# Kernel tuning notes

Hardware: AMD Instinct MI355X
Metric: run time of the kernel (lower is better)

## Reference

```python
import jax, jax.numpy as jnp
import numpy as np
import math

NEG_INF = -1e9  # stand-in for Const.NegInf
D_QKV = 64

def setup_inputs() -> dict:
    key = jax.random.key(0)
    kq, kk, kv, km = jax.random.split(key, 4)
    B, H, S, D = 4, 16, 2048, D_QKV
    q = jax.random.normal(kq, (B, H, S, D), dtype=jnp.float32)
    k = jax.random.normal(kk, (B, H, S, D), dtype=jnp.float32)
    v = jax.random.normal(kv, (B, H, S, D), dtype=jnp.float32)
    mask = jax.random.randint(km, (1, 1, S, S), 0, 2, dtype=jnp.int32)
    return {"q": q, "k": k, "v": v, "mask": mask, "batch": B, "q_seq": S}

def reference(q, k, v, mask, batch, q_seq):
    # scores: (B, H, Sq, Sk)
    scores = jnp.einsum('bhqd,bhkd->bhqk', q, k) / math.sqrt(D_QKV)
    # NOTE: non-standard order (faithful to source): log_softmax FIRST,
    # (dropout skipped since dropout_rate == 0), THEN post-softmax masking.
    score = jax.nn.log_softmax(scores, axis=-1)
    score = jnp.where(mask == 0, jnp.asarray(NEG_INF, score.dtype), score)
    att = jnp.einsum('bhqk,bhkd->bhqd', score, v)
    # (B, H, Sq, D) -> (B, Sq, H*D)
    return att.transpose(0, 2, 1, 3).reshape(batch, q_seq, -1)
```

## Files before the change

kernel.cpp:

```cpp
#include <hip/hip_runtime.h>

#define S_LEN 2048

typedef __attribute__((ext_vector_type(8))) short bf16x8;
typedef __attribute__((ext_vector_type(4))) float f32x4;
typedef __attribute__((ext_vector_type(4))) unsigned int u32x4;
typedef unsigned long long u64;
typedef unsigned int u32;
typedef unsigned short u16;

#define MFMA16 __builtin_amdgcn_mfma_f32_16x16x32_bf16

__device__ __forceinline__ u32 cvtpk(float a, float b) {
  u32 r;
  asm("v_cvt_pk_bf16_f32 %0, %1, %2" : "=v"(r) : "v"(a), "v"(b));
  return r;
}
__device__ __forceinline__ float exp2hw(float x) {
  float r;
  asm("v_exp_f32 %0, %1" : "=v"(r) : "v"(x));
  return r;
}

__device__ __forceinline__ u64* qkaddr(u16* dst, int row, int c4) {
  const int cb = c4 >> 1;
  return (u64*)((char*)dst + ((((row << 3) + (cb ^ (row & 7))) << 4) + ((c4 & 1) << 3)));
}
__device__ __forceinline__ bf16x8 ldfrag(const u16* base, int row, int blk) {
  const char* p = (const char*)base + (((row << 3) + (blk ^ (row & 7))) << 4);
  return *(const bf16x8*)p;
}

__device__ __forceinline__ void gload16(const u16* g, u16* l) {
  __builtin_amdgcn_global_load_lds((const __attribute__((address_space(1))) void*)g,
                                   (__attribute__((address_space(3))) void*)l, 16, 0, 0);
}

__global__ __launch_bounds__(256) void prep_kernel(
    const float* __restrict__ gk, const float* __restrict__ gv,
    const int* __restrict__ gmask,
    u16* __restrict__ wsK, u16* __restrict__ wsV,
    u16* __restrict__ wsM, float* __restrict__ wsVs) {
  __shared__ float tile[64 * 65];
  __shared__ float sred[2][256];
  const int bid = blockIdx.x, t = threadIdx.x;
  if (bid < 2048) {
    const int bh = bid >> 5, kt = bid & 31;
    const float* kg = gk + ((size_t)bh << 17) + ((size_t)kt << 12);
    const float* vg = gv + ((size_t)bh << 17) + ((size_t)kt << 12);
    u16* outK = wsK + ((size_t)bid << 12);
    u16* outV = wsV + ((size_t)bid << 12);
    const int r0 = t >> 4, c4 = t & 15;
#pragma unroll
    for (int i = 0; i < 4; ++i) {
      const int row = r0 + (i << 4);
      const float4 f = *(const float4*)(vg + (row << 6) + (c4 << 2));
      float* p = tile + row;
      p[((c4 << 2) + 0) * 65] = f.x;
      p[((c4 << 2) + 1) * 65] = f.y;
      p[((c4 << 2) + 2) * 65] = f.z;
      p[((c4 << 2) + 3) * 65] = f.w;
    }
#pragma unroll
    for (int i = 0; i < 2; ++i) {
      const int n = t + (i << 8);
      const int row = n >> 3, cb = (n & 7) ^ (row & 7);
      const float4 A = *(const float4*)(kg + (row << 6) + (cb << 3));
      const float4 B = *(const float4*)(kg + (row << 6) + (cb << 3) + 4);
      u32x4 w;
      w.x = cvtpk(A.x, A.y); w.y = cvtpk(A.z, A.w);
      w.z = cvtpk(B.x, B.y); w.w = cvtpk(B.z, B.w);
      *(u32x4*)(outK + ((size_t)n << 3)) = w;
    }
    __syncthreads();
#pragma unroll
    for (int i = 0; i < 2; ++i) {
      const int n = t + (i << 8);
      const int d = n >> 3, cb = (n & 7) ^ (d & 7);
      const float* src = tile + d * 65 + (cb << 3);
      float e[8], s = 0.f;
#pragma unroll
      for (int j = 0; j < 8; ++j) { e[j] = src[j]; s += e[j]; }
      sred[i][t] = s;
      u32x4 w;
      w.x = cvtpk(e[0], e[1]); w.y = cvtpk(e[2], e[3]);
      w.z = cvtpk(e[4], e[5]); w.w = cvtpk(e[6], e[7]);
      *(u32x4*)(outV + ((size_t)n << 3)) = w;
    }
    __syncthreads();
    if (t < 64) {
      const float* s8 = (t < 32) ? &sred[0][t << 3] : &sred[1][(t - 32) << 3];
      const float s = ((s8[0] + s8[1]) + (s8[2] + s8[3])) +
                      ((s8[4] + s8[5]) + (s8[6] + s8[7]));
      atomicAdd(&wsVs[(bh << 6) + t], s);
    }
  } else {
    const size_t base = ((size_t)(bid - 2048) << 12) + ((size_t)t << 4);
    int4 m[4];
#pragma unroll
    for (int i = 0; i < 4; ++i) m[i] = *(const int4*)(gmask + base + (i << 2));
    u32x4 w0, w1;
    w0.x = (m[0].x ? 0xFFFFu : 0u) | (m[0].y ? 0xFFFF0000u : 0u);
    w0.y = (m[0].z ? 0xFFFFu : 0u) | (m[0].w ? 0xFFFF0000u : 0u);
    w0.z = (m[1].x ? 0xFFFFu : 0u) | (m[1].y ? 0xFFFF0000u : 0u);
    w0.w = (m[1].z ? 0xFFFFu : 0u) | (m[1].w ? 0xFFFF0000u : 0u);
    w1.x = (m[2].x ? 0xFFFFu : 0u) | (m[2].y ? 0xFFFF0000u : 0u);
    w1.y = (m[2].z ? 0xFFFFu : 0u) | (m[2].w ? 0xFFFF0000u : 0u);
    w1.z = (m[3].x ? 0xFFFFu : 0u) | (m[3].y ? 0xFFFF0000u : 0u);
    w1.w = (m[3].z ? 0xFFFFu : 0u) | (m[3].w ? 0xFFFF0000u : 0u);
    *(u32x4*)(wsM + base) = w0;
    *(u32x4*)(wsM + base + 8) = w1;
  }
}

__global__ __launch_bounds__(256, 4) void attn_kernel(
    const float* __restrict__ gq, const u16* __restrict__ wsK,
    const u16* __restrict__ wsV, const u16* __restrict__ wsM,
    const float* __restrict__ wsVs, float* __restrict__ gout) {
  __shared__ __align__(16) u16 sK[2][4096];
  __shared__ __align__(16) u16 sV[2][4096];
  __shared__ __align__(16) u16 sW1[4096];

  const int t = threadIdx.x;
  const int wv = t >> 6;
  const int lane = t & 63;
  const int c = lane & 15;
  const int quad = lane >> 4;
  const int r0 = t >> 4, c4 = t & 15;

  const int bx = blockIdx.x;
  const int bh = bx & 63;
  const int q0 = (bx >> 6) << 6;

  const float* qg = gq + ((size_t)bh << 17) + ((size_t)q0 << 6);
  const u16* srcK = wsK + ((size_t)bh << 17) + (t << 3);
  const u16* srcV = wsV + ((size_t)bh << 17) + (t << 3);
  const int qrow = q0 + (wv << 4) + c;
  const u16* mrow = wsM + ((size_t)qrow << 11) + (quad << 3);

  f32x4 vreg[4];
#pragma unroll
  for (int mt = 0; mt < 4; ++mt)
    vreg[mt] = *(const f32x4*)(wsVs + (bh << 6) + (mt << 4) + (quad << 2));

  const float qs = 0.1803368801111204f;
#pragma unroll
  for (int i = 0; i < 4; ++i) {
    const int row = r0 + (i << 4);
    const float4 f = *(const float4*)(qg + ((size_t)row << 6) + (c4 << 2));
    const u32 lo = cvtpk(f.x * qs, f.y * qs);
    const u32 hi = cvtpk(f.z * qs, f.w * qs);
    *qkaddr(sW1, row, c4) = (u64)lo | ((u64)hi << 32);
  }
  __syncthreads();
  bf16x8 qf[2];
#pragma unroll
  for (int ks = 0; ks < 2; ++ks)
    qf[ks] = ldfrag(sW1, (wv << 4) + c, (ks << 2) + quad);
  asm volatile("s_waitcnt lgkmcnt(0)" ::: "memory");

  f32x4 accA[4], accB[4];
#pragma unroll
  for (int mt = 0; mt < 4; ++mt) {
    const f32x4 z = {0.f, 0.f, 0.f, 0.f};
    accA[mt] = z; accB[mt] = z;
  }
  float lacc = 0.f;

#define STAGE(kt_, buf_) do {                                        \
    const u16* sk_ = srcK + ((kt_) << 12);                           \
    const u16* sv_ = srcV + ((kt_) << 12);                           \
    u16* dk_ = &sK[buf_][wv << 9];                                   \
    u16* dv_ = &sV[buf_][wv << 9];                                   \
    gload16(sk_, dk_);                                               \
    gload16(sk_ + 2048, dk_ + 2048);                                 \
    gload16(sv_, dv_);                                               \
    gload16(sv_ + 2048, dv_ + 2048);                                 \
  } while (0)

  STAGE(0, 0);

  for (int kt = 0; kt < 32; ++kt) {
    const int cur = kt & 1;
    const u16* sKc = sK[cur];
    const u16* sVc = sV[cur];
    const u32x4 mm0 = *(const u32x4*)(mrow + ((size_t)kt << 6));
    const u32x4 mm1 = *(const u32x4*)(mrow + ((size_t)kt << 6) + 32);
    if (kt < 31) {
      STAGE(kt + 1, cur ^ 1);
      asm volatile("s_waitcnt vmcnt(6)" ::: "memory");
    } else {
      asm volatile("s_waitcnt vmcnt(2)" ::: "memory");
    }
    __builtin_amdgcn_s_barrier();
    asm volatile("" ::: "memory");

#pragma unroll
    for (int tr = 0; tr < 4; ++tr) {
      f32x4 acc = {0.f, 0.f, 0.f, 0.f};
      acc = MFMA16(ldfrag(sKc, (tr << 4) + c, quad), qf[0], acc, 0, 0, 0);
      acc = MFMA16(ldfrag(sKc, (tr << 4) + c, 4 + quad), qf[1], acc, 0, 0, 0);
      lacc += (exp2hw(acc[0]) + exp2hw(acc[1])) + (exp2hw(acc[2]) + exp2hw(acc[3]));
      *qkaddr(sW1, (wv << 4) + c, (tr << 2) + quad) =
          (u64)cvtpk(acc[0], acc[1]) | ((u64)cvtpk(acc[2], acc[3]) << 32);
    }
#pragma unroll
    for (int ks = 0; ks < 2; ++ks) {
      const u32x4 m = ks ? mm1 : mm0;
      const bf16x8 wr = ldfrag(sW1, (wv << 4) + c, (ks << 2) + quad);
      const u32x4 wraw = __builtin_bit_cast(u32x4, wr);
      const bf16x8 bw1 = __builtin_bit_cast(bf16x8, wraw & m);
      const bf16x8 bw2 = __builtin_bit_cast(bf16x8, m & 0x3F803F80u);
#pragma unroll
      for (int mt = 0; mt < 4; ++mt) {
        const bf16x8 av = ldfrag(sVc, (mt << 4) + c, (ks << 2) + quad);
        accA[mt] = MFMA16(av, bw1, accA[mt], 0, 0, 0);
        accB[mt] = MFMA16(av, bw2, accB[mt], 0, 0, 0);
      }
    }
    asm volatile("s_waitcnt lgkmcnt(0)" ::: "memory");
    __builtin_amdgcn_s_barrier();
  }
#undef STAGE

  float l = lacc;
  l += __shfl_xor(l, 16, 64);
  l += __shfl_xor(l, 32, 64);
  l = __log2f(l) * 0.6931471805599453f;
  const float c1 = 1e9f - l;

  const int b = bh >> 4, h = bh & 15;
  const float ln2 = 0.6931471805599453f;
#pragma unroll
  for (int mt = 0; mt < 4; ++mt) {
    float4 o;
    o.x = ln2 * accA[mt][0] + c1 * accB[mt][0] - 1e9f * vreg[mt][0];
    o.y = ln2 * accA[mt][1] + c1 * accB[mt][1] - 1e9f * vreg[mt][1];
    o.z = ln2 * accA[mt][2] + c1 * accB[mt][2] - 1e9f * vreg[mt][2];
    o.w = ln2 * accA[mt][3] + c1 * accB[mt][3] - 1e9f * vreg[mt][3];
    const size_t off = ((size_t)b * S_LEN + (size_t)qrow) * 1024 +
                       (h << 6) + (mt << 4) + (quad << 2);
    *(float4*)(gout + off) = o;
  }
}

extern "C" void kernel_launch(void* const* d_in, const int* in_sizes, int n_in,
                              void* d_out, int out_size, void* d_ws, size_t ws_size,
                              hipStream_t stream) {
  const float* q = (const float*)d_in[0];
  const float* k = (const float*)d_in[1];
  const float* v = (const float*)d_in[2];
  const int* mask = (const int*)d_in[3];
  (void)in_sizes; (void)n_in; (void)out_size; (void)ws_size;
  u16* wsK = (u16*)d_ws;
  u16* wsV = wsK + ((size_t)64 << 17);
  u16* wsM = wsV + ((size_t)64 << 17);
  float* wsVs = (float*)(wsM + ((size_t)S_LEN * S_LEN));
  hipMemsetAsync(wsVs, 0, 64 * 64 * sizeof(float), stream);
  prep_kernel<<<dim3(3072), dim3(256), 0, stream>>>(k, v, mask, wsK, wsV, wsM, wsVs);
  attn_kernel<<<dim3(2048), dim3(256), 0, stream>>>(q, wsK, wsV, wsM, wsVs, (float*)d_out);
}
```

Baseline: 295.5 us.

## Process 32 query rows per wave to reuse K/V tiles across two query groups

Each block now covers 128 query rows instead of 64, with each wave handling two 16-row query groups. K and V fragments loaded from LDS feed MFMAs for both groups, and the grid is halved, so K/V staging traffic per query is halved. Q is loaded straight into registers instead of going through LDS, and the score scratch becomes per-wave with its own swizzle. The QK and PV phases are interleaved in halves to overlap their work. The cost is twice the accumulator registers, which may lower occupancy under the 4-blocks-per-SM launch bound, and fewer blocks in the grid.

```diff
diff --git a/kernel.cpp b/kernel.cpp
--- a/kernel.cpp
+++ b/kernel.cpp
@@ -9,6 +9,9 @@
 typedef unsigned int u32;
 typedef unsigned short u16;
 
+typedef bf16x8 __attribute__((may_alias)) bf16x8a;
+typedef u64 __attribute__((may_alias)) u64a;
+
 #define MFMA16 __builtin_amdgcn_mfma_f32_16x16x32_bf16
 
 __device__ __forceinline__ u32 cvtpk(float a, float b) {
@@ -22,13 +25,9 @@
   return r;
 }
 
-__device__ __forceinline__ u64* qkaddr(u16* dst, int row, int c4) {
-  const int cb = c4 >> 1;
-  return (u64*)((char*)dst + ((((row << 3) + (cb ^ (row & 7))) << 4) + ((c4 & 1) << 3)));
-}
 __device__ __forceinline__ bf16x8 ldfrag(const u16* base, int row, int blk) {
   const char* p = (const char*)base + (((row << 3) + (blk ^ (row & 7))) << 4);
-  return *(const bf16x8*)p;
+  return *(const bf16x8a*)p;
 }
 
 __device__ __forceinline__ void gload16(const u16* g, u16* l) {
@@ -119,53 +118,48 @@
     const float* __restrict__ wsVs, float* __restrict__ gout) {
   __shared__ __align__(16) u16 sK[2][4096];
   __shared__ __align__(16) u16 sV[2][4096];
-  __shared__ __align__(16) u16 sW1[4096];
+  __shared__ __align__(16) u16 sW[4096];
 
   const int t = threadIdx.x;
   const int wv = t >> 6;
   const int lane = t & 63;
   const int c = lane & 15;
   const int quad = lane >> 4;
-  const int r0 = t >> 4, c4 = t & 15;
 
   const int bx = blockIdx.x;
   const int bh = bx & 63;
-  const int q0 = (bx >> 6) << 6;
+  const int q0 = (bx >> 6) << 7;
 
   const float* qg = gq + ((size_t)bh << 17) + ((size_t)q0 << 6);
   const u16* srcK = wsK + ((size_t)bh << 17) + (t << 3);
   const u16* srcV = wsV + ((size_t)bh << 17) + (t << 3);
-  const int qrow = q0 + (wv << 4) + c;
-  const u16* mrow = wsM + ((size_t)qrow << 11) + (quad << 3);
-
-  f32x4 vreg[4];
-#pragma unroll
-  for (int mt = 0; mt < 4; ++mt)
-    vreg[mt] = *(const f32x4*)(wsVs + (bh << 6) + (mt << 4) + (quad << 2));
+  const int qrow0 = q0 + (wv << 5) + c;
+  const u16* mrow0 = wsM + ((size_t)qrow0 << 11) + (quad << 3);
+  const u16* mrow1 = mrow0 + ((size_t)16 << 11);
+  u16* const wbase = sW + (wv << 10);
 
   const float qs = 0.1803368801111204f;
-#pragma unroll
-  for (int i = 0; i < 4; ++i) {
-    const int row = r0 + (i << 4);
-    const float4 f = *(const float4*)(qg + ((size_t)row << 6) + (c4 << 2));
-    const u32 lo = cvtpk(f.x * qs, f.y * qs);
-    const u32 hi = cvtpk(f.z * qs, f.w * qs);
-    *qkaddr(sW1, row, c4) = (u64)lo | ((u64)hi << 32);
-  }
-  __syncthreads();
-  bf16x8 qf[2];
-#pragma unroll
-  for (int ks = 0; ks < 2; ++ks)
-    qf[ks] = ldfrag(sW1, (wv << 4) + c, (ks << 2) + quad);
-  asm volatile("s_waitcnt lgkmcnt(0)" ::: "memory");
-
-  f32x4 accA[4], accB[4];
+  bf16x8 qf[2][2];
+#pragma unroll
+  for (int g = 0; g < 2; ++g)
+#pragma unroll
+    for (int s = 0; s < 2; ++s) {
+      const float* qp = qg + (((wv << 5) + (g << 4) + c) << 6) + (s << 5) + (quad << 3);
+      const float4 a = *(const float4*)qp;
+      const float4 b = *(const float4*)(qp + 4);
+      u32x4 w;
+      w.x = cvtpk(a.x * qs, a.y * qs); w.y = cvtpk(a.z * qs, a.w * qs);
+      w.z = cvtpk(b.x * qs, b.y * qs); w.w = cvtpk(b.z * qs, b.w * qs);
+      qf[g][s] = __builtin_bit_cast(bf16x8, w);
+    }
+
+  f32x4 accA0[4], accB0[4], accA1[4], accB1[4];
 #pragma unroll
   for (int mt = 0; mt < 4; ++mt) {
     const f32x4 z = {0.f, 0.f, 0.f, 0.f};
-    accA[mt] = z; accB[mt] = z;
-  }
-  float lacc = 0.f;
+    accA0[mt] = z; accB0[mt] = z; accA1[mt] = z; accB1[mt] = z;
+  }
+  float lac[2] = {0.f, 0.f};
 
 #define STAGE(kt_, buf_) do {                                        \
     const u16* sk_ = srcK + ((kt_) << 12);                           \
@@ -178,69 +172,112 @@
     gload16(sv_ + 2048, dv_ + 2048);                                 \
   } while (0)
 
+#define QK_STEP(tr_) do {                                                       \
+    const bf16x8 kf0 = ldfrag(sKc, ((tr_) << 4) + c, quad);                     \
+    const bf16x8 kf1 = ldfrag(sKc, ((tr_) << 4) + c, 4 + quad);                 \
+    _Pragma("unroll")                                                           \
+    for (int g = 0; g < 2; ++g) {                                               \
+      f32x4 acc = {0.f, 0.f, 0.f, 0.f};                                         \
+      acc = MFMA16(kf0, qf[g][0], acc, 0, 0, 0);                                \
+      acc = MFMA16(kf1, qf[g][1], acc, 0, 0, 0);                                \
+      lac[g] += (exp2hw(acc[0]) + exp2hw(acc[1])) +                             \
+                (exp2hw(acc[2]) + exp2hw(acc[3]));                              \
+      const int q_ = (g << 4) + c;                                              \
+      *(u64a*)((char*)wbase + (q_ << 6) +                                       \
+               ((((((tr_) & 1) << 1) + (quad >> 1)) ^ (q_ & 3)) << 4) +         \
+               ((quad & 1) << 3)) =                                             \
+          (u64)cvtpk(acc[0], acc[1]) | ((u64)cvtpk(acc[2], acc[3]) << 32);      \
+    }                                                                           \
+  } while (0)
+
+#define PV_STEP(ks_, m0_, m1_) do {                                             \
+    const u32x4 r0_ = __builtin_bit_cast(u32x4,                                 \
+        *(const bf16x8a*)((const char*)wbase + (c << 6) +                       \
+                          ((quad ^ (c & 3)) << 4)));                            \
+    const u32x4 r1_ = __builtin_bit_cast(u32x4,                                 \
+        *(const bf16x8a*)((const char*)wbase + ((16 + c) << 6) +                \
+                          ((quad ^ (c & 3)) << 4)));                            \
+    const bf16x8 w10 = __builtin_bit_cast(bf16x8, r0_ & (m0_));                 \
+    const bf16x8 w20 = __builtin_bit_cast(bf16x8, (m0_) & 0x3F803F80u);         \
+    const bf16x8 w11 = __builtin_bit_cast(bf16x8, r1_ & (m1_));                 \
+    const bf16x8 w21 = __builtin_bit_cast(bf16x8, (m1_) & 0x3F803F80u);         \
+    _Pragma("unroll")                                                           \
+    for (int mt = 0; mt < 4; ++mt) {                                            \
+      const bf16x8 av = ldfrag(sVc, (mt << 4) + c, ((ks_) << 2) + quad);        \
+      accA0[mt] = MFMA16(av, w10, accA0[mt], 0, 0, 0);                          \
+      accB0[mt] = MFMA16(av, w20, accB0[mt], 0, 0, 0);                          \
+      accA1[mt] = MFMA16(av, w11, accA1[mt], 0, 0, 0);                          \
+      accB1[mt] = MFMA16(av, w21, accB1[mt], 0, 0, 0);                          \
+    }                                                                           \
+  } while (0)
+
+#define MEMFENCE asm volatile("" ::: "memory")
+
   STAGE(0, 0);
 
   for (int kt = 0; kt < 32; ++kt) {
     const int cur = kt & 1;
     const u16* sKc = sK[cur];
     const u16* sVc = sV[cur];
-    const u32x4 mm0 = *(const u32x4*)(mrow + ((size_t)kt << 6));
-    const u32x4 mm1 = *(const u32x4*)(mrow + ((size_t)kt << 6) + 32);
+    const u32x4 m00 = *(const u32x4*)(mrow0 + (kt << 6));
+    const u32x4 m01 = *(const u32x4*)(mrow0 + (kt << 6) + 32);
+    const u32x4 m10 = *(const u32x4*)(mrow1 + (kt << 6));
+    const u32x4 m11 = *(const u32x4*)(mrow1 + (kt << 6) + 32);
     if (kt < 31) {
       STAGE(kt + 1, cur ^ 1);
-      asm volatile("s_waitcnt vmcnt(6)" ::: "memory");
+      asm volatile("s_waitcnt vmcnt(8)" ::: "memory");
     } else {
-      asm volatile("s_waitcnt vmcnt(2)" ::: "memory");
+      asm volatile("s_waitcnt vmcnt(4)" ::: "memory");
     }
     __builtin_amdgcn_s_barrier();
-    asm volatile("" ::: "memory");
-
-#pragma unroll
-    for (int tr = 0; tr < 4; ++tr) {
-      f32x4 acc = {0.f, 0.f, 0.f, 0.f};
-      acc = MFMA16(ldfrag(sKc, (tr << 4) + c, quad), qf[0], acc, 0, 0, 0);
-      acc = MFMA16(ldfrag(sKc, (tr << 4) + c, 4 + quad), qf[1], acc, 0, 0, 0);
-      lacc += (exp2hw(acc[0]) + exp2hw(acc[1])) + (exp2hw(acc[2]) + exp2hw(acc[3]));
-      *qkaddr(sW1, (wv << 4) + c, (tr << 2) + quad) =
-          (u64)cvtpk(acc[0], acc[1]) | ((u64)cvtpk(acc[2], acc[3]) << 32);
-    }
-#pragma unroll
-    for (int ks = 0; ks < 2; ++ks) {
-      const u32x4 m = ks ? mm1 : mm0;
-      const bf16x8 wr = ldfrag(sW1, (wv << 4) + c, (ks << 2) + quad);
-      const u32x4 wraw = __builtin_bit_cast(u32x4, wr);
-      const bf16x8 bw1 = __builtin_bit_cast(bf16x8, wraw & m);
-      const bf16x8 bw2 = __builtin_bit_cast(bf16x8, m & 0x3F803F80u);
-#pragma unroll
-      for (int mt = 0; mt < 4; ++mt) {
-        const bf16x8 av = ldfrag(sVc, (mt << 4) + c, (ks << 2) + quad);
-        accA[mt] = MFMA16(av, bw1, accA[mt], 0, 0, 0);
-        accB[mt] = MFMA16(av, bw2, accB[mt], 0, 0, 0);
-      }
-    }
+    MEMFENCE;
+
+    QK_STEP(0);
+    QK_STEP(1);
+    MEMFENCE;
+    PV_STEP(0, m00, m10);
+    MEMFENCE;
+    QK_STEP(2);
+    QK_STEP(3);
+    MEMFENCE;
+    PV_STEP(1, m01, m11);
+
     asm volatile("s_waitcnt lgkmcnt(0)" ::: "memory");
     __builtin_amdgcn_s_barrier();
   }
 #undef STAGE
-
-  float l = lacc;
-  l += __shfl_xor(l, 16, 64);
-  l += __shfl_xor(l, 32, 64);
-  l = __log2f(l) * 0.6931471805599453f;
-  const float c1 = 1e9f - l;
+#undef QK_STEP
+#undef PV_STEP
+#undef MEMFENCE
+
+  const float ln2 = 0.6931471805599453f;
+  float l0 = lac[0];
+  l0 += __shfl_xor(l0, 16, 64);
+  l0 += __shfl_xor(l0, 32, 64);
+  const float c10 = 1e9f - __log2f(l0) * ln2;
+  float l1 = lac[1];
+  l1 += __shfl_xor(l1, 16, 64);
+  l1 += __shfl_xor(l1, 32, 64);
+  const float c11 = 1e9f - __log2f(l1) * ln2;
 
   const int b = bh >> 4, h = bh & 15;
-  const float ln2 = 0.6931471805599453f;
 #pragma unroll
   for (int mt = 0; mt < 4; ++mt) {
+    const f32x4 vr = *(const f32x4*)(wsVs + (bh << 6) + (mt << 4) + (quad << 2));
     float4 o;
-    o.x = ln2 * accA[mt][0] + c1 * accB[mt][0] - 1e9f * vreg[mt][0];
-    o.y = ln2 * accA[mt][1] + c1 * accB[mt][1] - 1e9f * vreg[mt][1];
-    o.z = ln2 * accA[mt][2] + c1 * accB[mt][2] - 1e9f * vreg[mt][2];
-    o.w = ln2 * accA[mt][3] + c1 * accB[mt][3] - 1e9f * vreg[mt][3];
-    const size_t off = ((size_t)b * S_LEN + (size_t)qrow) * 1024 +
-                       (h << 6) + (mt << 4) + (quad << 2);
-    *(float4*)(gout + off) = o;
+    o.x = ln2 * accA0[mt][0] + c10 * accB0[mt][0] - 1e9f * vr[0];
+    o.y = ln2 * accA0[mt][1] + c10 * accB0[mt][1] - 1e9f * vr[1];
+    o.z = ln2 * accA0[mt][2] + c10 * accB0[mt][2] - 1e9f * vr[2];
+    o.w = ln2 * accA0[mt][3] + c10 * accB0[mt][3] - 1e9f * vr[3];
+    const size_t off0 = ((size_t)b * S_LEN + (size_t)qrow0) * 1024 +
+                        (h << 6) + (mt << 4) + (quad << 2);
+    *(float4*)(gout + off0) = o;
+    float4 p;
+    p.x = ln2 * accA1[mt][0] + c11 * accB1[mt][0] - 1e9f * vr[0];
+    p.y = ln2 * accA1[mt][1] + c11 * accB1[mt][1] - 1e9f * vr[1];
+    p.z = ln2 * accA1[mt][2] + c11 * accB1[mt][2] - 1e9f * vr[2];
+    p.w = ln2 * accA1[mt][3] + c11 * accB1[mt][3] - 1e9f * vr[3];
+    *(float4*)(gout + off0 + (16 << 10)) = p;
   }
 }
 
@@ -258,5 +295,5 @@
   float* wsVs = (float*)(wsM + ((size_t)S_LEN * S_LEN));
   hipMemsetAsync(wsVs, 0, 64 * 64 * sizeof(float), stream);
   prep_kernel<<<dim3(3072), dim3(256), 0, stream>>>(k, v, mask, wsK, wsV, wsM, wsVs);
-  attn_kernel<<<dim3(2048), dim3(256), 0, stream>>>(q, wsK, wsV, wsM, wsVs, (float*)d_out);
-}
+  attn_kernel<<<dim3(1024), dim3(256), 0, stream>>>(q, wsK, wsV, wsM, wsVs, (float*)d_out);
+}
```

Measured after the change: 440.6 us. +49.1%, slower.
